# Kernel tuning notes

Measured on AMD Instinct MI355X. Metric: run time of the kernel, lower is better.

Reference implementation:

```python
import jax, jax.numpy as jnp
import numpy as np

APP_DIM = 27
FEA_PE = 6
VIEW_PE = 6
FEATURE_C = 128
DENSITY_SHIFT = -10.0
DISTANCE_SCALE = 25.0
IN_MLPC = 2 * VIEW_PE * 3 + 2 * FEA_PE * APP_DIM + 3 + APP_DIM  # 390


def positional_encoding(x, freqs):
    # x: [..., C] -> [..., 2*freqs*C]
    freq_bands = (2.0 ** jnp.arange(freqs)).astype(x.dtype)
    pts = (x[..., None] * freq_bands).reshape(x.shape[:-1] + (freqs * x.shape[-1],))
    return jnp.concatenate([jnp.sin(pts), jnp.cos(pts)], axis=-1)


def alpha2weights(alpha):
    # alpha: [N_rays, N_samples]; last sample forced opaque (as in source)
    alpha = alpha.at[:, -1].set(1.0)
    trans = jnp.concatenate(
        [jnp.ones((alpha.shape[0], 1), alpha.dtype), 1.0 - alpha + 1e-10], axis=-1)
    T = jnp.cumprod(trans, axis=-1)
    weights = alpha * T[:, :-1]
    return weights, T


def setup_inputs() -> dict:
    key = jax.random.key(0)
    ks = jax.random.split(key, 12)
    N_rays, N_samples = 4096, 128
    sigma_feat = jax.random.normal(ks[0], (N_rays, N_samples), jnp.float32)
    app_features = 0.1 * jax.random.normal(ks[1], (N_rays, N_samples, APP_DIM), jnp.float32)
    vd = jax.random.normal(ks[2], (N_rays, N_samples, 3), jnp.float32)
    viewdirs = vd / (jnp.linalg.norm(vd, axis=-1, keepdims=True) + 1e-8)
    dists = 0.02 * jax.random.uniform(ks[3], (N_rays, N_samples), jnp.float32)

    def linear(k, fan_in, fan_out):
        kw, kb = jax.random.split(k)
        lim = 1.0 / np.sqrt(fan_in)
        W = jax.random.uniform(kw, (fan_in, fan_out), jnp.float32, -lim, lim)
        b = jax.random.uniform(kb, (fan_out,), jnp.float32, -lim, lim)
        return W, b

    W1, b1 = linear(ks[4], IN_MLPC, FEATURE_C)
    W2, b2 = linear(ks[5], FEATURE_C, FEATURE_C)
    W3, _ = linear(ks[6], FEATURE_C, 3)
    b3 = jnp.zeros((3,), jnp.float32)  # bias of last layer initialized to 0 in source
    return {"sigma_feat": sigma_feat, "app_features": app_features,
            "viewdirs": viewdirs, "dists": dists,
            "W1": W1, "b1": b1, "W2": W2, "b2": b2, "W3": W3, "b3": b3}


def reference(sigma_feat, app_features, viewdirs, dists, W1, b1, W2, b2, W3, b3):
    # feature2density: softplus with density_shift
    sigma = jax.nn.softplus(sigma_feat + DENSITY_SHIFT)
    alpha = 1.0 - jnp.exp(-sigma * dists * DISTANCE_SCALE)  # [N_rays, N_samples]
    weights, _T = alpha2weights(alpha)

    # MLPRender_Fea: cat[features, viewdirs, PE(features), PE(viewdirs)]
    mlp_in = jnp.concatenate(
        [app_features, viewdirs,
         positional_encoding(app_features, FEA_PE),
         positional_encoding(viewdirs, VIEW_PE)], axis=-1)  # [R, S, 390]
    h = jax.nn.relu(jnp.einsum('rsc,cf->rsf', mlp_in, W1) + b1)
    h = jax.nn.relu(jnp.einsum('rsf,fg->rsg', h, W2) + b2)
    rgb = jax.nn.sigmoid(jnp.einsum('rsg,go->rso', h, W3) + b3)  # [R, S, 3]

    rgb_map = jnp.sum(weights[..., None] * rgb, axis=-2)  # [R, 3]
    return rgb_map
```

## Files before the change

kernel.cpp:

```cpp
#include <hip/hip_runtime.h>
#include <math.h>

typedef unsigned short u16;
using bf16x8 = __attribute__((ext_vector_type(8))) short;
using f32x4  = __attribute__((ext_vector_type(4))) float;

#define NS      128
#define RAYS_PER_BLOCK 2
#define NBLOCKS (4096 / RAYS_PER_BLOCK)
#define KS1     15
#define NSLICE  19
#define XS      40

#define OW0   0
#define OW1   4096
#define OX0   8192
#define OX1   13312
#define OH1   8192
#define POOLSZ 24576

__device__ __forceinline__ u16 f2bf(float f) {
    unsigned int i = __float_as_uint(f);
    return (u16)((i + 0x7FFFu + ((i >> 16) & 1u)) >> 16);
}

__device__ __forceinline__ unsigned pk(float hi, float lo) {
    unsigned a = __float_as_uint(hi) + 0x8000u;
    unsigned b = __float_as_uint(lo) + 0x8000u;
    return __builtin_amdgcn_perm(a, b, 0x07060302u);
}
__device__ __forceinline__ u16 f2bf1(float f) {
    return (u16)((__float_as_uint(f) + 0x8000u) >> 16);
}

__device__ __forceinline__ int afoff(int m, int k) {
    return ((((k >> 5) * 8 + (m >> 4)) * 64) + (((k >> 3) & 3) * 16) + (m & 15)) * 8 + (k & 7);
}

__device__ __forceinline__ void stage_w(const u16* g, u16* l, int wave, int lane) {
    #pragma unroll
    for (int c = 0; c < 2; ++c) {
        const u16* gp = g + (wave * 2 + c) * 512 + lane * 8;
        u16* lp = l + (wave * 2 + c) * 512;
        __builtin_amdgcn_global_load_lds(
            (const __attribute__((address_space(1))) unsigned int*)gp,
            (__attribute__((address_space(3))) unsigned int*)lp, 16, 0, 0);
    }
}

__device__ __forceinline__ int orig_k(int ch, int slot) {
    if (ch < 27) {
        if (slot == 0) return ch;
        if (slot <= 6) return 30 + ch * 6 + (slot - 1);
        return 192 + ch * 6 + (slot - 7);
    } else {
        int c = ch - 27;
        if (slot == 0) return 27 + c;
        if (slot <= 6) return 354 + c * 6 + (slot - 1);
        return 372 + c * 6 + (slot - 7);
    }
}

__device__ __forceinline__ void build_x(u16* Xb, int m_b, int cl_b, float v) {
    float rev = v * 0.15915494309189535f;
    rev -= floorf(rev);
    float s0 = __builtin_amdgcn_sinf(rev);
    float c0 = __builtin_amdgcn_cosf(rev);
    float s1 = 2.f * s0 * c0, c1 = c0 * c0 - s0 * s0;
    float s2 = 2.f * s1 * c1, c2 = c1 * c1 - s1 * s1;
    float s3 = 2.f * s2 * c2, c3 = c2 * c2 - s2 * s2;
    float s4 = 2.f * s3 * c3, c4 = c3 * c3 - s3 * s3;
    float s5 = 2.f * s4 * c4, c5 = c4 * c4 - s4 * s4;
    uint4 lo, hi;
    lo.x = pk(s0, v);  lo.y = pk(s2, s1);  lo.z = pk(s4, s3);  lo.w = pk(c0, s5);
    hi.x = pk(c2, c1); hi.y = pk(c4, c3);  hi.z = pk(0.f, c5); hi.w = 0u;
    *(uint4*)(Xb + m_b * XS + cl_b * 16)     = lo;
    *(uint4*)(Xb + m_b * XS + cl_b * 16 + 8) = hi;
}

__global__ __launch_bounds__(256) void prep_kernel(
    const float* __restrict__ W1, const float* __restrict__ W2,
    const float* __restrict__ W3, u16* __restrict__ ws)
{
    int idx = blockIdx.x * 256 + threadIdx.x;
    if (idx < 61440) {
        int j = idx & 7, lane = (idx >> 3) & 63, nt = (idx >> 9) & 7, ks = idx >> 12;
        int q = lane >> 4, l15 = lane & 15;
        int klocal = q * 8 + j;
        int ch = ks * 2 + (klocal >> 4);
        int slot = klocal & 15;
        int n = nt * 16 + l15;
        ws[idx] = (slot < 13) ? f2bf(W1[orig_k(ch, slot) * 128 + n]) : (u16)0;
    } else if (idx < 77824) {
        int i2 = idx - 61440;
        int j = i2 & 7, lane = (i2 >> 3) & 63, nt = (i2 >> 9) & 7, ks = i2 >> 12;
        int k = ks * 32 + (lane >> 4) * 8 + j;
        int n = nt * 16 + (lane & 15);
        ws[idx] = f2bf(W2[k * 128 + n]);
    } else if (idx < 79872) {
        int i3 = idx - 77824;
        int j = i3 & 7, lane = (i3 >> 3) & 63, ks = i3 >> 9;
        int k = ks * 32 + (lane >> 4) * 8 + j;
        int n = lane & 15;
        ws[idx] = (n < 3) ? f2bf(W3[k * 3 + n]) : (u16)0;
    }
}

__global__ __launch_bounds__(256, 3) void render_kernel(
    const float* __restrict__ sigma_g, const float* __restrict__ app_g,
    const float* __restrict__ view_g,  const float* __restrict__ dists_g,
    const float* __restrict__ b1_g,    const float* __restrict__ b2_g,
    const float* __restrict__ b3_g,    const u16* __restrict__ ws,
    float* __restrict__ out_g)
{
    __shared__ __align__(16) u16 pool[POOLSZ];
    __shared__ float scanS;
    __shared__ float sum2[6];
    float* part = (float*)(pool + OW0);

    const int tid  = threadIdx.x;
    const int lane = tid & 63;
    const int wave = tid >> 6;
    const int l15  = lane & 15;
    const int quad = lane >> 4;
    const int wm   = wave >> 1;
    const int wn   = wave & 1;

    const u16* w3r = ws + 77824;

    float b1r[4], b2r[4];
    #pragma unroll
    for (int nt = 0; nt < 4; ++nt) {
        int col = wn * 64 + nt * 16 + l15;
        b1r[nt] = b1_g[col];
        b2r[nt] = b2_g[col];
    }
    const float b3v = (l15 < 3) ? b3_g[l15] : 0.f;
    bf16x8 w3fr[4];
    #pragma unroll
    for (int ks = 0; ks < 4; ++ks)
        w3fr[ks] = *(const bf16x8*)(w3r + (ks * 64 + lane) * 8);

    const int m_b  = tid >> 1;
    const int cl_b = tid & 1;

    #pragma unroll 1
    for (int ri = 0; ri < RAYS_PER_BLOCK; ++ri) {
        const int r  = blockIdx.x * RAYS_PER_BLOCK + ri;
        const int rb = r * NS;

        stage_w(ws, pool + OW0, wave, lane);

        float alpha = 0.f, prod = 1.f, wr = 0.f;
        if (tid < NS) {
            float x  = sigma_g[rb + tid] - 10.f;
            float sp = (x > 20.f) ? x : log1pf(expf(x));
            alpha = 1.f - expf(-sp * dists_g[rb + tid] * 25.f);
            if (tid == NS - 1) alpha = 1.f;
            float tb = 1.f - alpha + 1e-10f;
            prod = tb;
            #pragma unroll
            for (int d = 1; d < 64; d <<= 1) {
                float v = __shfl_up(prod, d);
                if (lane >= d) prod *= v;
            }
            if (tid == 63) scanS = prod;
        }

        build_x(pool + OX0, m_b, cl_b, app_g[(rb + m_b) * 27 + cl_b]);
        __syncthreads();

        if (tid < NS) {
            float prev = __shfl_up(prod, 1);
            float base = (lane == 0) ? 1.f : prev;
            float scale = (wave == 1) ? scanS : 1.f;
            wr = alpha * base * scale;
        }

        const f32x4 vzero = {0.f, 0.f, 0.f, 0.f};
        f32x4 acc[4][4];
        #pragma unroll
        for (int mt = 0; mt < 4; ++mt)
            #pragma unroll
            for (int nt = 0; nt < 4; ++nt) acc[mt][nt] = vzero;

        #pragma unroll 1
        for (int i = 0; i < NSLICE; ++i) {
            if (i + 1 < NSLICE)
                stage_w(ws + (i + 1) * 4096,
                        pool + ((((i + 1) & 1) == 0) ? OW0 : OW1), wave, lane);

            const u16* Wb = pool + (((i & 1) == 0) ? OW0 : OW1);
            bf16x8 a[4];
            if (i < KS1) {
                const u16* Xb = pool + (((i & 1) == 0) ? OX0 : OX1);
                #pragma unroll
                for (int mt = 0; mt < 4; ++mt)
                    a[mt] = *(const bf16x8*)(Xb + (wm * 64 + mt * 16 + l15) * XS + quad * 8);
            } else {
                const int i2 = i - KS1;
                #pragma unroll
                for (int mt = 0; mt < 4; ++mt)
                    a[mt] = *(const bf16x8*)(pool + OH1 +
                             ((i2 * 8 + wm * 4 + mt) * 64 + lane) * 8);
            }
            #pragma unroll
            for (int nt = 0; nt < 4; ++nt) {
                bf16x8 b = *(const bf16x8*)(Wb + ((wn * 4 + nt) * 64 + lane) * 8);
                #pragma unroll
                for (int mt = 0; mt < 4; ++mt)
                    acc[mt][nt] = __builtin_amdgcn_mfma_f32_16x16x32_bf16(a[mt], b, acc[mt][nt], 0, 0, 0);
            }
            if (i < KS1 - 1) {
                u16* Xb = pool + ((((i + 1) & 1) == 0) ? OX0 : OX1);
                int ch = 2 * (i + 1) + cl_b;
                float v = (ch < 27) ? app_g[(rb + m_b) * 27 + ch]
                                    : view_g[(rb + m_b) * 3 + (ch - 27)];
                build_x(Xb, m_b, cl_b, v);
            }
            if (i == KS1 - 1) {
                __syncthreads();
                #pragma unroll
                for (int mt = 0; mt < 4; ++mt)
                    #pragma unroll
                    for (int nt = 0; nt < 4; ++nt) {
                        int col = wn * 64 + nt * 16 + l15;
                        #pragma unroll
                        for (int rr = 0; rr < 4; ++rr) {
                            int row = wm * 64 + mt * 16 + quad * 4 + rr;
                            pool[OH1 + afoff(row, col)] =
                                f2bf1(fmaxf(acc[mt][nt][rr] + b1r[nt], 0.f));
                        }
                        acc[mt][nt] = vzero;
                    }
            }
            __syncthreads();
        }

        #pragma unroll
        for (int mt = 0; mt < 4; ++mt)
            #pragma unroll
            for (int nt = 0; nt < 4; ++nt) {
                int col = wn * 64 + nt * 16 + l15;
                #pragma unroll
                for (int rr = 0; rr < 4; ++rr) {
                    int row = wm * 64 + mt * 16 + quad * 4 + rr;
                    pool[OH1 + afoff(row, col)] =
                        f2bf1(fmaxf(acc[mt][nt][rr] + b2r[nt], 0.f));
                }
            }
        __syncthreads();

        f32x4 acc3[2] = {vzero, vzero};
        #pragma unroll
        for (int mi = 0; mi < 2; ++mi) {
            int mtt = wn * 2 + mi;
            #pragma unroll
            for (int ks = 0; ks < 4; ++ks) {
                bf16x8 a3 = *(const bf16x8*)(pool + OH1 +
                    ((ks * 8 + wm * 4 + mtt) * 64 + lane) * 8);
                acc3[mi] = __builtin_amdgcn_mfma_f32_16x16x32_bf16(a3, w3fr[ks], acc3[mi], 0, 0, 0);
            }
        }
        if (l15 < 3) {
            #pragma unroll
            for (int mi = 0; mi < 2; ++mi) {
                int mtt = wn * 2 + mi;
                #pragma unroll
                for (int rr = 0; rr < 4; ++rr) {
                    int row = wm * 64 + mtt * 16 + quad * 4 + rr;
                    float v = acc3[mi][rr] + b3v;
                    part[row * 3 + l15] = 1.f / (1.f + expf(-v));
                }
            }
        }
        __syncthreads();

        float v0 = 0.f, v1 = 0.f, v2 = 0.f;
        if (tid < NS) {
            v0 = wr * part[tid * 3 + 0];
            v1 = wr * part[tid * 3 + 1];
            v2 = wr * part[tid * 3 + 2];
            #pragma unroll
            for (int d = 1; d < 64; d <<= 1) {
                v0 += __shfl_xor(v0, d);
                v1 += __shfl_xor(v1, d);
                v2 += __shfl_xor(v2, d);
            }
            if (lane == 0) {
                sum2[wave * 3 + 0] = v0;
                sum2[wave * 3 + 1] = v1;
                sum2[wave * 3 + 2] = v2;
            }
        }
        __syncthreads();
        if (tid == 0) {
            out_g[r * 3 + 0] = sum2[0] + sum2[3];
            out_g[r * 3 + 1] = sum2[1] + sum2[4];
            out_g[r * 3 + 2] = sum2[2] + sum2[5];
        }
        __syncthreads();
    }
}

extern "C" void kernel_launch(void* const* d_in, const int* in_sizes, int n_in,
                              void* d_out, int out_size, void* d_ws, size_t ws_size,
                              hipStream_t stream) {
    (void)in_sizes; (void)n_in; (void)out_size; (void)ws_size;
    const float* sigma = (const float*)d_in[0];
    const float* app   = (const float*)d_in[1];
    const float* view  = (const float*)d_in[2];
    const float* dists = (const float*)d_in[3];
    const float* W1    = (const float*)d_in[4];
    const float* b1    = (const float*)d_in[5];
    const float* W2    = (const float*)d_in[6];
    const float* b2    = (const float*)d_in[7];
    const float* W3    = (const float*)d_in[8];
    const float* b3    = (const float*)d_in[9];
    float* out = (float*)d_out;

    u16* ws = (u16*)d_ws;

    prep_kernel<<<312, 256, 0, stream>>>(W1, W2, W3, ws);
    render_kernel<<<NBLOCKS, 256, 0, stream>>>(sigma, app, view, dists,
                                               b1, b2, b3, ws, out);
}
```

Measured before the change: 224.1 us.

## Store X tile in MFMA fragment layout and prefetch per-ray inputs into registers

Replaces the padded row-major X tile (stride 40) with a fragment-ordered layout, so the A operand loads use the same contiguous lane-indexed addressing as the hidden-layer tile. This unifies the two A-load paths. All 15 input channels per thread are also loaded from global memory into registers at the start of each ray, instead of one load inside each slice iteration. That takes global-load latency off the critical path of the MFMA loop, at the cost of extra register pressure.

```diff
diff --git a/kernel.cpp b/kernel.cpp
--- a/kernel.cpp
+++ b/kernel.cpp
@@ -10,12 +10,11 @@
 #define NBLOCKS (4096 / RAYS_PER_BLOCK)
 #define KS1     15
 #define NSLICE  19
-#define XS      40
 
 #define OW0   0
 #define OW1   4096
 #define OX0   8192
-#define OX1   13312
+#define OX1   12288
 #define OH1   8192
 #define POOLSZ 24576
 
@@ -74,8 +73,9 @@
     uint4 lo, hi;
     lo.x = pk(s0, v);  lo.y = pk(s2, s1);  lo.z = pk(s4, s3);  lo.w = pk(c0, s5);
     hi.x = pk(c2, c1); hi.y = pk(c4, c3);  hi.z = pk(0.f, c5); hi.w = 0u;
-    *(uint4*)(Xb + m_b * XS + cl_b * 16)     = lo;
-    *(uint4*)(Xb + m_b * XS + cl_b * 16 + 8) = hi;
+    int base = (m_b >> 4) * 512 + ((2 * cl_b) * 16 + (m_b & 15)) * 8;
+    *(uint4*)(Xb + base)       = lo;
+    *(uint4*)(Xb + base + 128) = hi;
 }
 
 __global__ __launch_bounds__(256) void prep_kernel(
@@ -149,6 +149,17 @@
         const int r  = blockIdx.x * RAYS_PER_BLOCK + ri;
         const int rb = r * NS;
 
+        float pv[15];
+        {
+            const float* ap = app_g  + (rb + m_b) * 27;
+            const float* vp = view_g + (rb + m_b) * 3;
+            #pragma unroll
+            for (int i = 0; i < 15; ++i) {
+                int ch = 2 * i + cl_b;
+                pv[i] = (ch < 27) ? ap[ch] : vp[ch - 27];
+            }
+        }
+
         stage_w(ws, pool + OW0, wave, lane);
 
         float alpha = 0.f, prod = 1.f, wr = 0.f;
@@ -167,7 +178,7 @@
             if (tid == 63) scanS = prod;
         }
 
-        build_x(pool + OX0, m_b, cl_b, app_g[(rb + m_b) * 27 + cl_b]);
+        build_x(pool + OX0, m_b, cl_b, pv[0]);
         __syncthreads();
 
         if (tid < NS) {
@@ -191,19 +202,13 @@
                         pool + ((((i + 1) & 1) == 0) ? OW0 : OW1), wave, lane);
 
             const u16* Wb = pool + (((i & 1) == 0) ? OW0 : OW1);
+            const u16* Asrc = (i < KS1)
+                ? (pool + (((i & 1) == 0) ? OX0 : OX1))
+                : (pool + OH1 + (i - KS1) * 4096);
             bf16x8 a[4];
-            if (i < KS1) {
-                const u16* Xb = pool + (((i & 1) == 0) ? OX0 : OX1);
-                #pragma unroll
-                for (int mt = 0; mt < 4; ++mt)
-                    a[mt] = *(const bf16x8*)(Xb + (wm * 64 + mt * 16 + l15) * XS + quad * 8);
-            } else {
-                const int i2 = i - KS1;
-                #pragma unroll
-                for (int mt = 0; mt < 4; ++mt)
-                    a[mt] = *(const bf16x8*)(pool + OH1 +
-                             ((i2 * 8 + wm * 4 + mt) * 64 + lane) * 8);
-            }
+            #pragma unroll
+            for (int mt = 0; mt < 4; ++mt)
+                a[mt] = *(const bf16x8*)(Asrc + ((wm * 4 + mt) * 64 + lane) * 8);
             #pragma unroll
             for (int nt = 0; nt < 4; ++nt) {
                 bf16x8 b = *(const bf16x8*)(Wb + ((wn * 4 + nt) * 64 + lane) * 8);
@@ -213,10 +218,7 @@
             }
             if (i < KS1 - 1) {
                 u16* Xb = pool + ((((i + 1) & 1) == 0) ? OX0 : OX1);
-                int ch = 2 * (i + 1) + cl_b;
-                float v = (ch < 27) ? app_g[(rb + m_b) * 27 + ch]
-                                    : view_g[(rb + m_b) * 3 + (ch - 27)];
-                build_x(Xb, m_b, cl_b, v);
+                build_x(Xb, m_b, cl_b, pv[i + 1]);
             }
             if (i == KS1 - 1) {
                 __syncthreads();
@@ -257,8 +259,8 @@
             int mtt = wn * 2 + mi;
             #pragma unroll
             for (int ks = 0; ks < 4; ++ks) {
-                bf16x8 a3 = *(const bf16x8*)(pool + OH1 +
-                    ((ks * 8 + wm * 4 + mtt) * 64 + lane) * 8);
+                bf16x8 a3 = *(const bf16x8*)(pool + OH1 + ks * 4096 +
+                    ((wm * 4 + mtt) * 64 + lane) * 8);
                 acc3[mi] = __builtin_amdgcn_mfma_f32_16x16x32_bf16(a3, w3fr[ks], acc3[mi], 0, 0, 0);
             }
         }
```

Result: no change. 226.9 us (+1.3%).
